# Performance work log

Measured on AMD Instinct MI355X. Metric: run time of the kernel, lower is better.

The kernel has to match this reference:

```python
import jax, jax.numpy as jnp
import numpy as np

B, IMG, P, CIN, D, L, H, HID = 64, 224, 16, 3, 768, 12, 12, 3072
HD = D // H                      # 64 head dim
N = (IMG // P) ** 2 + 1          # 197 tokens (cls + patches)
EQ = 1.0 / np.sqrt(D)            # EqualLinear scale (lr_mul=1)


def _ln(x):
    # LayerNorm(eps=1e-3, elementwise_affine=False)
    m = jnp.mean(x, axis=-1, keepdims=True)
    v = jnp.var(x, axis=-1, keepdims=True)
    return (x - m) * jax.lax.rsqrt(v + 1e-3)


def _smln(x, latent, gw, gb, bw, bb):
    # SelfModulatedLayerNorm: param-free LN then per-sample affine from latent
    gamma = (latent @ (gw * EQ).T + gb)[:, None, :]
    beta = (latent @ (bw * EQ).T + bb)[:, None, :]
    return _ln(x) * (1.0 + gamma) + beta


def _attention(x, qkvw, projw, projb):
    b, n, d = x.shape
    qkv = (x @ qkvw.T).reshape(b, n, 3, H, HD).transpose(2, 0, 3, 1, 4)  # [3,B,H,N,hd]
    q, k, v = qkv[0], qkv[1], qkv[2]
    attn = jax.nn.softmax(jnp.einsum('bhqd,bhkd->bhqk', q, k) * (HD ** -0.5), axis=-1)
    out = jnp.einsum('bhqk,bhkd->bhqd', attn, v).transpose(0, 2, 1, 3).reshape(b, n, d)
    return out @ projw.T + projb


def _forward(x, latent, conv_w, conv_b, cls_token, pos_embed,
             g1w, g1b, b1w, b1b, qkvw, projw, projb,
             g2w, g2b, b2w, b2b, fc1w, fc1b, fc2w, fc2b,
             gnw, gnb, bnw, bnb):
    b = x.shape[0]
    # PatchEmbed: conv stride=patch, flatten, transpose, sin activation
    feat = jax.lax.conv_general_dilated(
        x, conv_w, (P, P), 'VALID',
        dimension_numbers=('NCHW', 'OIHW', 'NCHW')) + conv_b[None, :, None, None]
    tok = jnp.sin(feat.reshape(b, D, -1).transpose(0, 2, 1))          # [B,196,D]
    tok = jnp.concatenate([jnp.broadcast_to(cls_token, (b, 1, D)), tok], axis=1)
    tok = tok + pos_embed                                             # [B,197,D]

    def block(t, p):
        (g1w_, g1b_, b1w_, b1b_, qkvw_, projw_, projb_,
         g2w_, g2b_, b2w_, b2b_, fc1w_, fc1b_, fc2w_, fc2b_) = p
        xn = _smln(t, latent, g1w_, g1b_, b1w_, b1b_)
        y = _attention(xn, qkvw_, projw_, projb_) + xn
        t = xn + y                       # source Block: x reassigned to norm1 output
        t = _smln(t, latent, g2w_, g2b_, b2w_, b2b_)
        h = jax.nn.gelu(t @ fc1w_.T + fc1b_, approximate=False)
        t = (h @ fc2w_.T + fc2b_) + t
        return t, None

    tok, _ = jax.lax.scan(block, tok, (g1w, g1b, b1w, b1b, qkvw, projw, projb,
                                       g2w, g2b, b2w, b2b, fc1w, fc1b, fc2w, fc2b))
    return _smln(tok, latent, gnw, gnb, bnw, bnb)


def setup_inputs() -> dict:
    key = jax.random.key(0)
    ks = jax.random.split(key, 20)
    r = lambda k, shape: 0.02 * jax.random.normal(k, shape, dtype=jnp.float32)
    z = lambda shape: jnp.zeros(shape, jnp.float32)
    return {
        'x': jax.random.normal(ks[0], (B, CIN, IMG, IMG), dtype=jnp.float32),
        'latent': jax.random.normal(ks[1], (B, D), dtype=jnp.float32),
        'conv_w': r(ks[2], (D, CIN, P, P)), 'conv_b': z((D,)),
        'cls_token': z((1, 1, D)), 'pos_embed': r(ks[3], (1, N, D)),
        'g1w': r(ks[4], (L, D, D)), 'g1b': z((L, D)),
        'b1w': r(ks[5], (L, D, D)), 'b1b': z((L, D)),
        'qkvw': r(ks[6], (L, 3 * D, D)),
        'projw': r(ks[7], (L, D, D)), 'projb': z((L, D)),
        'g2w': r(ks[8], (L, D, D)), 'g2b': z((L, D)),
        'b2w': r(ks[9], (L, D, D)), 'b2b': z((L, D)),
        'fc1w': r(ks[10], (L, HID, D)), 'fc1b': z((L, HID)),
        'fc2w': r(ks[11], (L, D, HID)), 'fc2b': z((L, D)),
        'gnw': r(ks[12], (D, D)), 'gnb': z((D,)),
        'bnw': r(ks[13], (D, D)), 'bnb': z((D,)),
    }


def reference(x, latent, conv_w, conv_b, cls_token, pos_embed,
              g1w, g1b, b1w, b1b, qkvw, projw, projb,
              g2w, g2b, b2w, b2b, fc1w, fc1b, fc2w, fc2b,
              gnw, gnb, bnw, bnb):
    return _forward(x, latent, conv_w, conv_b, cls_token, pos_embed,
                    g1w, g1b, b1w, b1b, qkvw, projw, projb,
                    g2w, g2b, b2w, b2b, fc1w, fc1b, fc2w, fc2b,
                    gnw, gnb, bnw, bnb)
```

## Files before the change

kernel.cpp:

```cpp
#include <hip/hip_runtime.h>

typedef unsigned short u16;
typedef __bf16 bf16x8 __attribute__((ext_vector_type(8)));
typedef unsigned short u16x8 __attribute__((ext_vector_type(8)));
typedef float f32x4 __attribute__((ext_vector_type(4)));

#define B_    64
#define NTOK  197
#define DIM   768
#define NH    12
#define LAY   12
#define HID_  3072
#define MROWS (B_*NTOK)

#define EPI_BF16  0
#define EPI_PROJ  2
#define EPI_GELU  3
#define EPI_FC2   4
#define EPI_PATCH 5

__device__ __forceinline__ u16 f2bf(float f) {
  unsigned u = __float_as_uint(f);
  u += 0x7FFFu + ((u >> 16) & 1u);
  return (u16)(u >> 16);
}
__device__ __forceinline__ float bf2f(u16 h) {
  return __uint_as_float(((unsigned)h) << 16);
}

__device__ __forceinline__ void gld_lds16(const void* g, void* l) {
  __builtin_amdgcn_global_load_lds(
      (const __attribute__((address_space(1))) void*)g,
      (__attribute__((address_space(3))) void*)l, 16, 0, 0);
}

__global__ void fill_k(float* __restrict__ o, float v, int n) {
  int i = blockIdx.x * blockDim.x + threadIdx.x;
  const int st = gridDim.x * blockDim.x;
  for (; i < n; i += st) o[i] = v;
}

__global__ void cvt_bf16(const float* __restrict__ in, u16* __restrict__ out, int n4) {
  int i = blockIdx.x * blockDim.x + threadIdx.x;
  const int st = gridDim.x * blockDim.x;
  for (; i < n4; i += st) {
    float4 v = ((const float4*)in)[i];
    ushort4 o;
    o.x = f2bf(v.x); o.y = f2bf(v.y); o.z = f2bf(v.z); o.w = f2bf(v.w);
    ((ushort4*)out)[i] = o;
  }
}

__global__ void cvt4_k(const float* __restrict__ s0, const float* __restrict__ s1,
                       const float* __restrict__ s2, const float* __restrict__ s3,
                       u16* __restrict__ d0, u16* __restrict__ d1,
                       u16* __restrict__ d2, u16* __restrict__ d3,
                       int n0, int n1, int n2, int n3)
{
  int i = blockIdx.x * blockDim.x + threadIdx.x;
  const int st = gridDim.x * blockDim.x;
  const int total = n0 + n1 + n2 + n3;
  for (; i < total; i += st) {
    const float* s; u16* d; int j = i;
    if (j < n0) { s = s0; d = d0; }
    else { j -= n0;
      if (j < n1) { s = s1; d = d1; }
      else { j -= n1;
        if (j < n2) { s = s2; d = d2; }
        else { j -= n2; s = s3; d = d3; } } }
    float4 v = ((const float4*)s)[j];
    ushort4 o;
    o.x = f2bf(v.x); o.y = f2bf(v.y); o.z = f2bf(v.z); o.w = f2bf(v.w);
    ((ushort4*)d)[j] = o;
  }
}

__global__ void im2col_k(const float* __restrict__ x, u16* __restrict__ out) {
  int i = blockIdx.x * blockDim.x + threadIdx.x;
  const int st = gridDim.x * blockDim.x;
  const int total = 12544 * 768;
  for (; i < total; i += st) {
    int row = i / 768, col = i - row * 768;
    int b = row / 196, pr = row - b * 196;
    int py = pr / 14, px = pr - py * 14;
    int cin = col >> 8, rr = col & 255;
    int ky = rr >> 4, kx = rr & 15;
    out[i] = f2bf(x[((b * 3 + cin) * 224 + py * 16 + ky) * 224 + px * 16 + kx]);
  }
}

__global__ void clspos_k(const float* __restrict__ cls, const float* __restrict__ pos,
                         float* __restrict__ t) {
  int i = blockIdx.x * blockDim.x + threadIdx.x;
  if (i >= B_ * DIM) return;
  int b = i / DIM, d = i - b * DIM;
  t[(size_t)b * NTOK * DIM + d] = cls[d] + pos[d];
}

__global__ __launch_bounds__(256)
void modk(const float* __restrict__ lat, const float* __restrict__ w,
          const float* __restrict__ bias, float* __restrict__ out, int ldb)
{
  __shared__ float ls[32][65];
  __shared__ float wsm[64][33];
  const int tid = threadIdx.x;
  const int mat = blockIdx.y;
  const int n0 = blockIdx.x * 64;
  const int nl = tid & 63;
  const int bg = tid >> 6;
  float acc[16];
  #pragma unroll
  for (int j = 0; j < 16; ++j) acc[j] = 0.f;
  for (int k0 = 0; k0 < 768; k0 += 32) {
    __syncthreads();
    #pragma unroll
    for (int i = 0; i < 8; ++i) {
      int idx = tid + i * 256;
      int rr = idx >> 5, kk = idx & 31;
      ls[kk][rr]  = lat[rr * 768 + k0 + kk];
      wsm[rr][kk] = w[((size_t)mat * 768 + n0 + rr) * 768 + k0 + kk];
    }
    __syncthreads();
    #pragma unroll 4
    for (int kk = 0; kk < 32; ++kk) {
      float wv = wsm[nl][kk];
      #pragma unroll
      for (int j = 0; j < 16; ++j)
        acc[j] += ls[kk][bg * 16 + j] * wv;
    }
  }
  const float EQS = 0.036084391824351615f;
  const float* bs = bias + (size_t)mat * 768 + n0;
  #pragma unroll
  for (int j = 0; j < 16; ++j) {
    int b = bg * 16 + j;
    out[(size_t)b * ldb + mat * 768 + n0 + nl] = acc[j] * EQS + bs[nl];
  }
}

__global__ __launch_bounds__(256)
void smln_k(const float* __restrict__ x,
            const float* __restrict__ gamma, const float* __restrict__ beta, int ldg,
            float* __restrict__ oF, u16* __restrict__ oB)
{
  const int row = blockIdx.x;
  const int tid = threadIdx.x;
  const float* xr = x + (size_t)row * DIM;
  float v0 = xr[tid], v1 = xr[tid + 256], v2 = xr[tid + 512];
  float s1 = v0 + v1 + v2;
  float s2 = v0 * v0 + v1 * v1 + v2 * v2;
  #pragma unroll
  for (int o = 32; o; o >>= 1) { s1 += __shfl_xor(s1, o); s2 += __shfl_xor(s2, o); }
  __shared__ float rs[8];
  const int lane = tid & 63, wv = tid >> 6;
  if (lane == 0) { rs[wv] = s1; rs[4 + wv] = s2; }
  __syncthreads();
  s1 = rs[0] + rs[1] + rs[2] + rs[3];
  s2 = rs[4] + rs[5] + rs[6] + rs[7];
  const float mean = s1 * (1.f / 768.f);
  const float var  = s2 * (1.f / 768.f) - mean * mean;
  const float rstd = rsqrtf(var + 1e-3f);
  const int b = row / NTOK;
  const float* g  = gamma + (size_t)b * ldg;
  const float* be = beta  + (size_t)b * ldg;
  const size_t base = (size_t)row * DIM;
  float vv[3] = {v0, v1, v2};
  #pragma unroll
  for (int j = 0; j < 3; ++j) {
    int d = tid + j * 256;
    float y = (vv[j] - mean) * rstd;
    y = y * (1.f + g[d]) + be[d];
    oF[base + d] = y;
    if (oB) oB[base + d] = f2bf(y);
  }
}

__global__ __launch_bounds__(256)
void attn_k(const u16* __restrict__ qkv, u16* __restrict__ ao)
{
  __shared__ u16 Ks[208 * 68];
  __shared__ u16 Vt[64 * 226];
  __shared__ u16 Ps[4][16 * 228];
  const int bh = blockIdx.x;
  const int b = bh / NH, h = bh - (bh / NH) * NH;
  const int tid = threadIdx.x;
  const int lane = tid & 63, wv = tid >> 6;
  const int lr = lane & 15, kg = lane >> 4;
  const size_t tb = (size_t)(b * NTOK) * 2304 + h * 64;

  for (int t = tid; t < 1576; t += 256) {
    int n = t >> 3, c = t & 7;
    *(u16x8*)&Ks[n * 68 + c * 8] =
        *(const u16x8*)&qkv[tb + (size_t)n * 2304 + 768 + c * 8];
  }
  for (int t = tid; t < 1576; t += 256) {
    int n = t >> 3, dc = t & 7;
    u16x8 v = *(const u16x8*)&qkv[tb + (size_t)n * 2304 + 1536 + dc * 8];
    #pragma unroll
    for (int j = 0; j < 8; ++j) Vt[(dc * 8 + j) * 226 + n] = v[j];
  }
  for (int i = tid; i < 11 * 68; i += 256) Ks[197 * 68 + i] = 0;
  for (int i = tid; i < 64 * 29; i += 256) {
    int d = i / 29, c = i - d * 29;
    Vt[d * 226 + 197 + c] = 0;
  }
  for (int i = tid; i < 4 * 16 * 20; i += 256) {
    int w = i / 320, rm = i - w * 320, r = rm / 20, c = rm - r * 20;
    Ps[w][r * 228 + 208 + c] = 0;
  }
  __syncthreads();

  const f32x4 z4 = {0.f, 0.f, 0.f, 0.f};
  u16* pw = Ps[wv];

  for (int qt = wv; qt < 13; qt += 4) {
    const int q0 = qt * 16;
    const int qrow = min(q0 + lr, 196);
    const bf16x8 aq0 = *(const bf16x8*)&qkv[tb + (size_t)qrow * 2304 + kg * 8];
    const bf16x8 aq1 = *(const bf16x8*)&qkv[tb + (size_t)qrow * 2304 + 32 + kg * 8];

    f32x4 acc[13];
    #pragma unroll
    for (int ct = 0; ct < 13; ++ct) acc[ct] = z4;
    #pragma unroll
    for (int ct = 0; ct < 13; ++ct) {
      const bf16x8 bk0 = *(const bf16x8*)&Ks[(ct * 16 + lr) * 68 + kg * 8];
      const bf16x8 bk1 = *(const bf16x8*)&Ks[(ct * 16 + lr) * 68 + 32 + kg * 8];
      acc[ct] = __builtin_amdgcn_mfma_f32_16x16x32_bf16(aq0, bk0, acc[ct], 0, 0, 0);
      acc[ct] = __builtin_amdgcn_mfma_f32_16x16x32_bf16(aq1, bk1, acc[ct], 0, 0, 0);
    }

    float mx[4], sm[4], inv[4];
    #pragma unroll
    for (int r = 0; r < 4; ++r) mx[r] = -1e30f;
    #pragma unroll
    for (int ct = 0; ct < 13; ++ct)
      #pragma unroll
      for (int r = 0; r < 4; ++r) {
        float s = acc[ct][r] * 0.125f;
        if (ct * 16 + lr >= 197) s = -1e30f;
        acc[ct][r] = s;
        mx[r] = fmaxf(mx[r], s);
      }
    #pragma unroll
    for (int o = 1; o < 16; o <<= 1)
      #pragma unroll
      for (int r = 0; r < 4; ++r) mx[r] = fmaxf(mx[r], __shfl_xor(mx[r], o));
    #pragma unroll
    for (int r = 0; r < 4; ++r) sm[r] = 0.f;
    #pragma unroll
    for (int ct = 0; ct < 13; ++ct)
      #pragma unroll
      for (int r = 0; r < 4; ++r) {
        float p = __expf(acc[ct][r] - mx[r]);
        acc[ct][r] = p;
        sm[r] += p;
      }
    #pragma unroll
    for (int o = 1; o < 16; o <<= 1)
      #pragma unroll
      for (int r = 0; r < 4; ++r) sm[r] += __shfl_xor(sm[r], o);
    #pragma unroll
    for (int r = 0; r < 4; ++r) inv[r] = 1.f / sm[r];

    #pragma unroll
    for (int ct = 0; ct < 13; ++ct)
      #pragma unroll
      for (int r = 0; r < 4; ++r)
        pw[(kg * 4 + r) * 228 + ct * 16 + lr] = f2bf(acc[ct][r]);
    asm volatile("s_waitcnt lgkmcnt(0)" ::: "memory");
    __builtin_amdgcn_sched_barrier(0);

    f32x4 accO[4];
    #pragma unroll
    for (int dt = 0; dt < 4; ++dt) accO[dt] = z4;
    #pragma unroll
    for (int kt = 0; kt < 7; ++kt) {
      const bf16x8 ap = *(const bf16x8*)&pw[lr * 228 + kt * 32 + kg * 8];
      #pragma unroll
      for (int dt = 0; dt < 4; ++dt) {
        const bf16x8 bv = *(const bf16x8*)&Vt[(dt * 16 + lr) * 226 + kt * 32 + kg * 8];
        accO[dt] = __builtin_amdgcn_mfma_f32_16x16x32_bf16(ap, bv, accO[dt], 0, 0, 0);
      }
    }

    #pragma unroll
    for (int r = 0; r < 4; ++r) {
      const int q = q0 + kg * 4 + r;
      if (q < NTOK) {
        const size_t base = ((size_t)(b * NTOK + q)) * DIM + h * 64;
        #pragma unroll
        for (int dt = 0; dt < 4; ++dt)
          ao[base + dt * 16 + lr] = f2bf(accO[dt][r] * inv[r]);
      }
    }
  }
}

template<int EPI>
__global__ __launch_bounds__(256)
void gemm_bt(const u16* __restrict__ A, int lda,
             const u16* __restrict__ Bw, int ldb,
             int M, int K, int gn,
             const float* __restrict__ bias,
             const float* __restrict__ res,
             float* __restrict__ outF, u16* __restrict__ outB, int ldo,
             const float* __restrict__ aux)
{
  __shared__ u16 SA[3][4096];
  __shared__ u16 SB[3][4096];
  const int tid = threadIdx.x;
  const int lane = tid & 63, wv = tid >> 6;
  const int lr = lane & 15, kg = lane >> 4;
  const int wm = wv >> 1, wn = wv & 1;

  const int nwg = gridDim.x;
  const int qq = nwg >> 3, rr2 = nwg & 7;
  const int xcd = blockIdx.x & 7, loc = blockIdx.x >> 3;
  const int v = (xcd < rr2 ? xcd * (qq + 1) : rr2 * (qq + 1) + (xcd - rr2) * qq) + loc;
  const int tm = v / gn, tn = v - tm * gn;

  const int c0 = tid, c1 = tid + 256;
  const int r0 = c0 >> 2, q0 = (c0 & 3) ^ (r0 & 3) ^ ((r0 >> 2) & 3);
  const int r1 = c1 >> 2, q1 = (c1 & 3) ^ (r1 & 3) ^ ((r1 >> 2) & 3);
  int am0 = tm * 128 + r0; if (am0 >= M) am0 = M - 1;
  int am1 = tm * 128 + r1; if (am1 >= M) am1 = M - 1;
  const u16* aS0 = A  + (size_t)am0 * lda + q0 * 8;
  const u16* aS1 = A  + (size_t)am1 * lda + q1 * 8;
  const u16* bS0 = Bw + (size_t)(tn * 128 + r0) * ldb + q0 * 8;
  const u16* bS1 = Bw + (size_t)(tn * 128 + r1) * ldb + q1 * 8;

  f32x4 acc[4][4];
  const f32x4 z = {0.f, 0.f, 0.f, 0.f};
  #pragma unroll
  for (int m = 0; m < 4; ++m)
    #pragma unroll
    for (int n = 0; n < 4; ++n) acc[m][n] = z;

#define STG(buf, ko) do { \
    u16* aD = &SA[buf][wv * 512]; u16* bD = &SB[buf][wv * 512]; \
    gld_lds16(aS0 + (ko), aD);        gld_lds16(aS1 + (ko), aD + 2048); \
    gld_lds16(bS0 + (ko), bD);        gld_lds16(bS1 + (ko), bD + 2048); \
  } while (0)

  const int KT = K >> 5;
  STG(0, 0);
  STG(1, 32);
  asm volatile("s_waitcnt vmcnt(4)" ::: "memory");
  __builtin_amdgcn_s_barrier();
  __builtin_amdgcn_sched_barrier(0);

  for (int t = 0; t < KT; ++t) {
    const int buf = t % 3;
    if (t) {
      asm volatile("s_waitcnt lgkmcnt(0)" ::: "memory");
      __builtin_amdgcn_sched_barrier(0);
      if (t + 1 < KT) asm volatile("s_waitcnt vmcnt(4)" ::: "memory");
      else            asm volatile("s_waitcnt vmcnt(0)" ::: "memory");
      __builtin_amdgcn_s_barrier();
      __builtin_amdgcn_sched_barrier(0);
    }
    if (t + 2 < KT) STG((t + 2) % 3, (t + 2) * 32);
    bf16x8 af[4], bfr[4];
    #pragma unroll
    for (int m = 0; m < 4; ++m) {
      int row = wm * 64 + m * 16 + lr;
      af[m] = *(const bf16x8*)&SA[buf][row * 32 + (((kg ^ row ^ (row >> 2)) & 3) << 3)];
    }
    #pragma unroll
    for (int n = 0; n < 4; ++n) {
      int row = wn * 64 + n * 16 + lr;
      bfr[n] = *(const bf16x8*)&SB[buf][row * 32 + (((kg ^ row ^ (row >> 2)) & 3) << 3)];
    }
    #pragma unroll
    for (int m = 0; m < 4; ++m)
      #pragma unroll
      for (int n = 0; n < 4; ++n)
        acc[m][n] = __builtin_amdgcn_mfma_f32_16x16x32_bf16(af[m], bfr[n], acc[m][n], 0, 0, 0);
  }
#undef STG
  __syncthreads();

  const int gr0 = tm * 128 + wm * 64;
  const int gc0 = tn * 128 + wn * 64;
  if constexpr (EPI == EPI_BF16 || EPI == EPI_GELU) {
    u16* T = (u16*)SA + wv * 1152;
    #pragma unroll
    for (int m = 0; m < 4; ++m) {
      #pragma unroll
      for (int n = 0; n < 4; ++n) {
        #pragma unroll
        for (int r = 0; r < 4; ++r) {
          float val = acc[m][n][r];
          if constexpr (EPI == EPI_GELU) {
            float u = val + bias[gc0 + n * 16 + lr];
            val = 0.5f * u * (1.f + erff(u * 0.70710678118654752f));
          }
          T[(kg * 4 + r) * 72 + n * 16 + lr] = f2bf(val);
        }
      }
      asm volatile("s_waitcnt lgkmcnt(0)" ::: "memory");
      __builtin_amdgcn_sched_barrier(0);
      #pragma unroll
      for (int half = 0; half < 2; ++half) {
        int row = (lane >> 3) + half * 8;
        int c8 = lane & 7;
        u16x8 vv = *(const u16x8*)&T[row * 72 + c8 * 8];
        int gr = gr0 + m * 16 + row;
        if (gr < M) *(u16x8*)&outB[(size_t)gr * ldo + gc0 + c8 * 8] = vv;
      }
      asm volatile("s_waitcnt lgkmcnt(0)" ::: "memory");
      __builtin_amdgcn_sched_barrier(0);
    }
  } else {
    float* T = (float*)SA + wv * 1088;
    #pragma unroll
    for (int m = 0; m < 4; ++m) {
      #pragma unroll
      for (int n = 0; n < 4; ++n)
        #pragma unroll
        for (int r = 0; r < 4; ++r)
          T[(kg * 4 + r) * 68 + n * 16 + lr] = acc[m][n][r];
      asm volatile("s_waitcnt lgkmcnt(0)" ::: "memory");
      __builtin_amdgcn_sched_barrier(0);
      #pragma unroll
      for (int qu = 0; qu < 4; ++qu) {
        int row = (lane >> 4) + qu * 4;
        int c4 = lane & 15;
        f32x4 vv = *(const f32x4*)&T[row * 68 + c4 * 4];
        int gr = gr0 + m * 16 + row;
        int gc = gc0 + c4 * 4;
        if (gr < M) {
          f32x4 bv = *(const f32x4*)&bias[gc];
          if constexpr (EPI == EPI_PROJ) {
            size_t o = (size_t)gr * ldo + gc;
            f32x4 rv = *(const f32x4*)&res[o];
            f32x4 ov = vv + bv + 2.f * rv;
            *(f32x4*)&outF[o] = ov;
          } else if constexpr (EPI == EPI_FC2) {
            size_t o = (size_t)gr * ldo + gc;
            f32x4 rv = *(const f32x4*)&res[o];
            f32x4 ov = vv + bv + rv;
            *(f32x4*)&outF[o] = ov;
          } else {
            int pb = gr / 196, pp = gr - pb * 196;
            size_t o = ((size_t)pb * NTOK + 1 + pp) * DIM + gc;
            f32x4 av = *(const f32x4*)&aux[(size_t)(1 + pp) * DIM + gc];
            f32x4 ov;
            #pragma unroll
            for (int j = 0; j < 4; ++j) ov[j] = sinf(vv[j] + bv[j]) + av[j];
            *(f32x4*)&outF[o] = ov;
          }
        }
      }
      asm volatile("s_waitcnt lgkmcnt(0)" ::: "memory");
      __builtin_amdgcn_sched_barrier(0);
    }
  }
}

extern "C" void kernel_launch(void* const* d_in, const int* in_sizes, int n_in,
                              void* d_out, int out_size, void* d_ws, size_t ws_size,
                              hipStream_t stream)
{
  (void)in_sizes; (void)n_in;
  const float* X     = (const float*)d_in[0];
  const float* LAT   = (const float*)d_in[1];
  const float* CONVW = (const float*)d_in[2];
  const float* CONVB = (const float*)d_in[3];
  const float* CLS   = (const float*)d_in[4];
  const float* POS   = (const float*)d_in[5];
  const float* G1W   = (const float*)d_in[6];
  const float* G1B   = (const float*)d_in[7];
  const float* B1W   = (const float*)d_in[8];
  const float* B1B   = (const float*)d_in[9];
  const float* QKVW  = (const float*)d_in[10];
  const float* PROJW = (const float*)d_in[11];
  const float* PROJB = (const float*)d_in[12];
  const float* G2W   = (const float*)d_in[13];
  const float* G2B   = (const float*)d_in[14];
  const float* B2W   = (const float*)d_in[15];
  const float* B2B   = (const float*)d_in[16];
  const float* FC1W  = (const float*)d_in[17];
  const float* FC1B  = (const float*)d_in[18];
  const float* FC2W  = (const float*)d_in[19];
  const float* FC2B  = (const float*)d_in[20];
  const float* GNW   = (const float*)d_in[21];
  const float* GNB   = (const float*)d_in[22];
  const float* BNW   = (const float*)d_in[23];
  const float* BNB   = (const float*)d_in[24];

  char* p = (char*)d_ws;
  auto carve = [&](size_t bytes) { char* r = p; p += (bytes + 255) & ~(size_t)255; return r; };

  char* Ubuf  = carve((size_t)MROWS * HID_ * 2);
  u16* patches = (u16*)Ubuf;
  u16* qkvb    = (u16*)Ubuf;
  u16* hb      = (u16*)Ubuf;
  u16* wconv  = (u16*)carve((size_t)768 * 768 * 2);
  u16* wqkv_l = (u16*)carve((size_t)2304 * 768 * 2);
  u16* wproj_l= (u16*)carve((size_t)768 * 768 * 2);
  u16* wfc1_l = (u16*)carve((size_t)3072 * 768 * 2);
  u16* wfc2_l = (u16*)carve((size_t)768 * 3072 * 2);
  float* tf   = (float*)carve((size_t)MROWS * 768 * 4);
  float* xnf  = (float*)carve((size_t)MROWS * 768 * 4);
  u16* xnb    = (u16*)carve((size_t)MROWS * 768 * 2);
  u16* aob    = (u16*)carve((size_t)MROWS * 768 * 2);
  float* gam1 = (float*)carve((size_t)B_ * 9216 * 4);
  float* bet1 = (float*)carve((size_t)B_ * 9216 * 4);
  float* gam2 = (float*)carve((size_t)B_ * 9216 * 4);
  float* bet2 = (float*)carve((size_t)B_ * 9216 * 4);
  float* gamN = (float*)carve((size_t)B_ * 768 * 4);
  float* betN = (float*)carve((size_t)B_ * 768 * 4);

  fill_k<<<1, 64, 0, stream>>>((float*)d_out, 1e9f, 1);
  if ((size_t)(p - (char*)d_ws) > ws_size) {
    fill_k<<<256, 256, 0, stream>>>((float*)d_out, 1e9f, out_size);
    return;
  }

  modk<<<dim3(12, 12), 256, 0, stream>>>(LAT, G1W, G1B, gam1, 9216);
  modk<<<dim3(12, 12), 256, 0, stream>>>(LAT, B1W, B1B, bet1, 9216);
  modk<<<dim3(12, 12), 256, 0, stream>>>(LAT, G2W, G2B, gam2, 9216);
  modk<<<dim3(12, 12), 256, 0, stream>>>(LAT, B2W, B2B, bet2, 9216);
  modk<<<dim3(12, 1),  256, 0, stream>>>(LAT, GNW, GNB, gamN, 768);
  modk<<<dim3(12, 1),  256, 0, stream>>>(LAT, BNW, BNB, betN, 768);

  {
    int n4 = 768 * 768 / 4;
    cvt_bf16<<<(n4 + 255) / 256, 256, 0, stream>>>(CONVW, wconv, n4);
  }
  im2col_k<<<4096, 256, 0, stream>>>(X, patches);
  gemm_bt<EPI_PATCH><<<98 * 6, 256, 0, stream>>>(patches, 768, wconv, 768, 12544, 768, 6,
                                                 CONVB, nullptr, tf, nullptr, 768, POS);
  clspos_k<<<(B_ * DIM + 255) / 256, 256, 0, stream>>>(CLS, POS, tf);

  const int n4_qkv = 2304 * 768 / 4, n4_pro = 768 * 768 / 4, n4_fc = 3072 * 768 / 4;
  for (int l = 0; l < LAY; ++l) {
    cvt4_k<<<4096, 256, 0, stream>>>(QKVW + (size_t)l * 2304 * 768, PROJW + (size_t)l * 768 * 768,
                                     FC1W + (size_t)l * 3072 * 768, FC2W + (size_t)l * 768 * 3072,
                                     wqkv_l, wproj_l, wfc1_l, wfc2_l,
                                     n4_qkv, n4_pro, n4_fc, n4_fc);
    smln_k<<<MROWS, 256, 0, stream>>>(tf, gam1 + l * 768, bet1 + l * 768, 9216, xnf, xnb);
    gemm_bt<EPI_BF16><<<99 * 18, 256, 0, stream>>>(xnb, 768, wqkv_l, 768, MROWS, 768, 18,
                                                   nullptr, nullptr, nullptr, qkvb, 2304, nullptr);
    attn_k<<<B_ * NH, 256, 0, stream>>>(qkvb, aob);
    gemm_bt<EPI_PROJ><<<99 * 6, 256, 0, stream>>>(aob, 768, wproj_l, 768, MROWS, 768, 6,
                                                  PROJB + l * 768, xnf, tf, nullptr, 768, nullptr);
    smln_k<<<MROWS, 256, 0, stream>>>(tf, gam2 + l * 768, bet2 + l * 768, 9216, xnf, xnb);
    gemm_bt<EPI_GELU><<<99 * 24, 256, 0, stream>>>(xnb, 768, wfc1_l, 768, MROWS, 768, 24,
                                                   FC1B + l * 3072, nullptr, nullptr, hb, 3072, nullptr);
    gemm_bt<EPI_FC2><<<99 * 6, 256, 0, stream>>>(hb, 3072, wfc2_l, 3072, MROWS, 3072, 6,
                                                 FC2B + l * 768, xnf, tf, nullptr, 768, nullptr);
  }
  smln_k<<<MROWS, 256, 0, stream>>>(tf, gamN, betN, 768, (float*)d_out, nullptr);
}
```

Measured before the change: 6.069 ms.

## Add 256x256-tile 8-wave GEMM for QKV and FC1, unroll triple-buffer loop

Adds a new GEMM kernel with 512 threads and 256x256 output tiles, a K-step of 64, double-buffered LDS and a phased schedule. The phases interleave A-fragment reads, global-to-LDS prefetch and MFMA bursts raised with s_setprio. The QKV and FC1 GEMMs use it, which cuts global/LDS traffic per FLOP and the number of workgroups. The existing 128x128 GEMM's main loop is also unrolled by three so buffer indices become compile-time constants instead of t%3. Risks: 256-row tiles waste work on the last M tile (12608 rows), fewer blocks means less occupancy and tail balance, and the 64KB of LDS per block limits co-residency. The unrolled loop steps by three and does not guard t < KT inside the body, so it relies on KT being a multiple of three, which holds for K=768 and K=3072.

```diff
diff --git a/kernel.cpp b/kernel.cpp
--- a/kernel.cpp
+++ b/kernel.cpp
@@ -298,6 +298,149 @@
 }
 
 template<int EPI>
+__global__ __launch_bounds__(512, 2)
+void gemm8(const u16* __restrict__ A, int lda,
+           const u16* __restrict__ Bw, int ldb,
+           int M, int K, int gn,
+           const float* __restrict__ bias,
+           u16* __restrict__ outB, int ldo)
+{
+  __shared__ u16 SA[2][16384];
+  __shared__ u16 SB[2][16384];
+  const int tid = threadIdx.x;
+  const int lane = tid & 63, wv = tid >> 6;
+  const int lr = lane & 15, kg = lane >> 4;
+  const int wm = wv >> 2, wn = wv & 3;
+
+  const int nwg = gridDim.x;
+  const int qq = nwg >> 3, rr2 = nwg & 7;
+  const int xcd = blockIdx.x & 7, loc = blockIdx.x >> 3;
+  const int v = (xcd < rr2 ? xcd * (qq + 1) : rr2 * (qq + 1) + (xcd - rr2) * qq) + loc;
+  const int tm = v / gn, tn = v - tm * gn;
+
+  const u16* aSrc[4];
+  const u16* bSrc[4];
+  #pragma unroll
+  for (int j = 0; j < 4; ++j) {
+    const int c = tid + j * 512;
+    const int r = c >> 3, q = (c & 7) ^ (r & 7);
+    int am = tm * 256 + r; if (am >= M) am = M - 1;
+    aSrc[j] = A  + (size_t)am * lda + q * 8;
+    bSrc[j] = Bw + (size_t)(tn * 256 + r) * ldb + q * 8;
+  }
+
+  f32x4 acc[8][4];
+  const f32x4 z = {0.f, 0.f, 0.f, 0.f};
+  #pragma unroll
+  for (int m = 0; m < 8; ++m)
+    #pragma unroll
+    for (int n = 0; n < 4; ++n) acc[m][n] = z;
+
+  const int KT = K >> 6;
+  #pragma unroll
+  for (int j = 0; j < 4; ++j) {
+    gld_lds16(aSrc[j], &SA[0][(tid + j * 512) * 8]);
+    gld_lds16(bSrc[j], &SB[0][(tid + j * 512) * 8]);
+  }
+  asm volatile("s_waitcnt vmcnt(0)" ::: "memory");
+  __builtin_amdgcn_s_barrier();
+  __builtin_amdgcn_sched_barrier(0);
+
+#define G8_PHASE(p) do { \
+    bf16x8 af[2][2]; \
+    _Pragma("unroll") \
+    for (int ks = 0; ks < 2; ++ks) \
+      _Pragma("unroll") \
+      for (int mm = 0; mm < 2; ++mm) { \
+        const int rrow = wm * 128 + ((p) * 2 + mm) * 16 + lr; \
+        af[ks][mm] = *(const bf16x8*)&sa[rrow * 64 + ((((ks * 4 + kg) ^ (rrow & 7))) << 3)]; \
+      } \
+    if ((p) < 2 && pf) { \
+      const int j0 = (p) * 2, j1 = (p) * 2 + 1; \
+      gld_lds16(aSrc[j0] + ko, &san[(tid + j0 * 512) * 8]); \
+      gld_lds16(aSrc[j1] + ko, &san[(tid + j1 * 512) * 8]); \
+      gld_lds16(bSrc[j0] + ko, &sbn[(tid + j0 * 512) * 8]); \
+      gld_lds16(bSrc[j1] + ko, &sbn[(tid + j1 * 512) * 8]); \
+    } \
+    __builtin_amdgcn_s_barrier(); \
+    asm volatile("s_waitcnt lgkmcnt(0)" ::: "memory"); \
+    __builtin_amdgcn_sched_barrier(0); \
+    __builtin_amdgcn_s_setprio(1); \
+    _Pragma("unroll") \
+    for (int ks = 0; ks < 2; ++ks) \
+      _Pragma("unroll") \
+      for (int mm = 0; mm < 2; ++mm) \
+        _Pragma("unroll") \
+        for (int n = 0; n < 4; ++n) \
+          acc[(p) * 2 + mm][n] = __builtin_amdgcn_mfma_f32_16x16x32_bf16( \
+              af[ks][mm], bfr[ks][n], acc[(p) * 2 + mm][n], 0, 0, 0); \
+    __builtin_amdgcn_s_setprio(0); \
+  } while (0)
+
+  for (int kt = 0; kt < KT; ++kt) {
+    const int bu = kt & 1;
+    const u16* sa = SA[bu];
+    const u16* sb = SB[bu];
+    u16* san = SA[bu ^ 1];
+    u16* sbn = SB[bu ^ 1];
+    const int ko = (kt + 1) * 64;
+    const bool pf = (kt + 1 < KT);
+
+    bf16x8 bfr[2][4];
+    #pragma unroll
+    for (int ks = 0; ks < 2; ++ks)
+      #pragma unroll
+      for (int n = 0; n < 4; ++n) {
+        const int rrow = wn * 64 + n * 16 + lr;
+        bfr[ks][n] = *(const bf16x8*)&sb[rrow * 64 + ((((ks * 4 + kg) ^ (rrow & 7))) << 3)];
+      }
+
+    G8_PHASE(0);
+    __builtin_amdgcn_s_barrier();
+    G8_PHASE(1);
+    __builtin_amdgcn_s_barrier();
+    G8_PHASE(2);
+    __builtin_amdgcn_s_barrier();
+    G8_PHASE(3);
+    if (pf) { asm volatile("s_waitcnt vmcnt(0)" ::: "memory"); }
+    __builtin_amdgcn_s_barrier();
+    __builtin_amdgcn_sched_barrier(0);
+  }
+#undef G8_PHASE
+
+  const int gr0 = tm * 256 + wm * 128;
+  const int gc0 = tn * 256 + wn * 64;
+  u16* T = (u16*)SA + wv * 1152;
+  #pragma unroll
+  for (int m = 0; m < 8; ++m) {
+    #pragma unroll
+    for (int n = 0; n < 4; ++n) {
+      #pragma unroll
+      for (int r = 0; r < 4; ++r) {
+        float val = acc[m][n][r];
+        if constexpr (EPI == EPI_GELU) {
+          float u = val + bias[gc0 + n * 16 + lr];
+          val = 0.5f * u * (1.f + erff(u * 0.70710678118654752f));
+        }
+        T[(kg * 4 + r) * 72 + n * 16 + lr] = f2bf(val);
+      }
+    }
+    asm volatile("s_waitcnt lgkmcnt(0)" ::: "memory");
+    __builtin_amdgcn_sched_barrier(0);
+    #pragma unroll
+    for (int half = 0; half < 2; ++half) {
+      int row = (lane >> 3) + half * 8;
+      int c8 = lane & 7;
+      u16x8 vv = *(const u16x8*)&T[row * 72 + c8 * 8];
+      int gr = gr0 + m * 16 + row;
+      if (gr < M) *(u16x8*)&outB[(size_t)gr * ldo + gc0 + c8 * 8] = vv;
+    }
+    asm volatile("s_waitcnt lgkmcnt(0)" ::: "memory");
+    __builtin_amdgcn_sched_barrier(0);
+  }
+}
+
+template<int EPI>
 __global__ __launch_bounds__(256)
 void gemm_bt(const u16* __restrict__ A, int lda,
              const u16* __restrict__ Bw, int ldb,
@@ -350,33 +493,37 @@
   __builtin_amdgcn_s_barrier();
   __builtin_amdgcn_sched_barrier(0);
 
-  for (int t = 0; t < KT; ++t) {
-    const int buf = t % 3;
-    if (t) {
-      asm volatile("s_waitcnt lgkmcnt(0)" ::: "memory");
-      __builtin_amdgcn_sched_barrier(0);
-      if (t + 1 < KT) asm volatile("s_waitcnt vmcnt(4)" ::: "memory");
-      else            asm volatile("s_waitcnt vmcnt(0)" ::: "memory");
-      __builtin_amdgcn_s_barrier();
-      __builtin_amdgcn_sched_barrier(0);
-    }
-    if (t + 2 < KT) STG((t + 2) % 3, (t + 2) * 32);
-    bf16x8 af[4], bfr[4];
-    #pragma unroll
-    for (int m = 0; m < 4; ++m) {
-      int row = wm * 64 + m * 16 + lr;
-      af[m] = *(const bf16x8*)&SA[buf][row * 32 + (((kg ^ row ^ (row >> 2)) & 3) << 3)];
-    }
-    #pragma unroll
-    for (int n = 0; n < 4; ++n) {
-      int row = wn * 64 + n * 16 + lr;
-      bfr[n] = *(const bf16x8*)&SB[buf][row * 32 + (((kg ^ row ^ (row >> 2)) & 3) << 3)];
-    }
-    #pragma unroll
-    for (int m = 0; m < 4; ++m)
-      #pragma unroll
-      for (int n = 0; n < 4; ++n)
-        acc[m][n] = __builtin_amdgcn_mfma_f32_16x16x32_bf16(af[m], bfr[n], acc[m][n], 0, 0, 0);
+  #pragma unroll 1
+  for (int t0 = 0; t0 < KT; t0 += 3) {
+    #pragma unroll
+    for (int u = 0; u < 3; ++u) {
+      const int t = t0 + u;
+      if (t) {
+        asm volatile("s_waitcnt lgkmcnt(0)" ::: "memory");
+        __builtin_amdgcn_sched_barrier(0);
+        if (t + 1 < KT) asm volatile("s_waitcnt vmcnt(4)" ::: "memory");
+        else            asm volatile("s_waitcnt vmcnt(0)" ::: "memory");
+        __builtin_amdgcn_s_barrier();
+        __builtin_amdgcn_sched_barrier(0);
+      }
+      if (t + 2 < KT) STG((u + 2) % 3, (t + 2) * 32);
+      bf16x8 af[4], bfr[4];
+      #pragma unroll
+      for (int m = 0; m < 4; ++m) {
+        int row = wm * 64 + m * 16 + lr;
+        af[m] = *(const bf16x8*)&SA[u][row * 32 + (((kg ^ row ^ (row >> 2)) & 3) << 3)];
+      }
+      #pragma unroll
+      for (int n = 0; n < 4; ++n) {
+        int row = wn * 64 + n * 16 + lr;
+        bfr[n] = *(const bf16x8*)&SB[u][row * 32 + (((kg ^ row ^ (row >> 2)) & 3) << 3)];
+      }
+      #pragma unroll
+      for (int m = 0; m < 4; ++m)
+        #pragma unroll
+        for (int n = 0; n < 4; ++n)
+          acc[m][n] = __builtin_amdgcn_mfma_f32_16x16x32_bf16(af[m], bfr[n], acc[m][n], 0, 0, 0);
+    }
   }
 #undef STG
   __syncthreads();
@@ -542,14 +689,14 @@
                                      wqkv_l, wproj_l, wfc1_l, wfc2_l,
                                      n4_qkv, n4_pro, n4_fc, n4_fc);
     smln_k<<<MROWS, 256, 0, stream>>>(tf, gam1 + l * 768, bet1 + l * 768, 9216, xnf, xnb);
-    gemm_bt<EPI_BF16><<<99 * 18, 256, 0, stream>>>(xnb, 768, wqkv_l, 768, MROWS, 768, 18,
-                                                   nullptr, nullptr, nullptr, qkvb, 2304, nullptr);
+    gemm8<EPI_BF16><<<50 * 9, 512, 0, stream>>>(xnb, 768, wqkv_l, 768, MROWS, 768, 9,
+                                                nullptr, qkvb, 2304);
     attn_k<<<B_ * NH, 256, 0, stream>>>(qkvb, aob);
     gemm_bt<EPI_PROJ><<<99 * 6, 256, 0, stream>>>(aob, 768, wproj_l, 768, MROWS, 768, 6,
                                                   PROJB + l * 768, xnf, tf, nullptr, 768, nullptr);
     smln_k<<<MROWS, 256, 0, stream>>>(tf, gam2 + l * 768, bet2 + l * 768, 9216, xnf, xnb);
-    gemm_bt<EPI_GELU><<<99 * 24, 256, 0, stream>>>(xnb, 768, wfc1_l, 768, MROWS, 768, 24,
-                                                   FC1B + l * 3072, nullptr, nullptr, hb, 3072, nullptr);
+    gemm8<EPI_GELU><<<50 * 12, 512, 0, stream>>>(xnb, 768, wfc1_l, 768, MROWS, 768, 12,
+                                                 FC1B + l * 3072, hb, 3072);
     gemm_bt<EPI_FC2><<<99 * 6, 256, 0, stream>>>(hb, 3072, wfc2_l, 3072, MROWS, 3072, 6,
                                                  FC2B + l * 768, xnf, tf, nullptr, 768, nullptr);
   }
```

Measured after the change: 7.652 ms. 26.1% more time.

## Drop fp32 norm output, read bf16 residual, add 4-stage GEMM pipeline option

Applied to the files above, without the earlier changes.

The layer-norm kernels stop writing the fp32 normalized activations, and the proj and fc2 epilogues read the residual from the bf16 copy instead. This cuts activation memory traffic per layer. The GEMM gains a templated pipeline depth, with the K loop unrolled by depth, and the QKV and FC1 GEMMs use 4 LDS stages. The risks are lower residual precision from the bf16 rounding, and higher LDS use, which may lower occupancy.

```diff
diff --git a/kernel.cpp b/kernel.cpp
--- a/kernel.cpp
+++ b/kernel.cpp
@@ -170,7 +170,7 @@
     int d = tid + j * 256;
     float y = (vv[j] - mean) * rstd;
     y = y * (1.f + g[d]) + be[d];
-    oF[base + d] = y;
+    if (oF) oF[base + d] = y;
     if (oB) oB[base + d] = f2bf(y);
   }
 }
@@ -297,18 +297,18 @@
   }
 }
 
-template<int EPI>
+template<int EPI, int DEPTH>
 __global__ __launch_bounds__(256)
 void gemm_bt(const u16* __restrict__ A, int lda,
              const u16* __restrict__ Bw, int ldb,
              int M, int K, int gn,
              const float* __restrict__ bias,
-             const float* __restrict__ res,
+             const u16* __restrict__ res,
              float* __restrict__ outF, u16* __restrict__ outB, int ldo,
              const float* __restrict__ aux)
 {
-  __shared__ u16 SA[3][4096];
-  __shared__ u16 SB[3][4096];
+  __shared__ u16 SA[DEPTH][4096];
+  __shared__ u16 SB[DEPTH][4096];
   const int tid = threadIdx.x;
   const int lane = tid & 63, wv = tid >> 6;
   const int lr = lane & 15, kg = lane >> 4;
@@ -344,39 +344,50 @@
   } while (0)
 
   const int KT = K >> 5;
-  STG(0, 0);
-  STG(1, 32);
-  asm volatile("s_waitcnt vmcnt(4)" ::: "memory");
+  #pragma unroll
+  for (int d = 0; d < DEPTH - 1; ++d) STG(d, d * 32);
+  if constexpr (DEPTH == 4) { asm volatile("s_waitcnt vmcnt(8)" ::: "memory"); }
+  else                      { asm volatile("s_waitcnt vmcnt(4)" ::: "memory"); }
   __builtin_amdgcn_s_barrier();
   __builtin_amdgcn_sched_barrier(0);
 
-  for (int t = 0; t < KT; ++t) {
-    const int buf = t % 3;
-    if (t) {
-      asm volatile("s_waitcnt lgkmcnt(0)" ::: "memory");
-      __builtin_amdgcn_sched_barrier(0);
-      if (t + 1 < KT) asm volatile("s_waitcnt vmcnt(4)" ::: "memory");
-      else            asm volatile("s_waitcnt vmcnt(0)" ::: "memory");
-      __builtin_amdgcn_s_barrier();
-      __builtin_amdgcn_sched_barrier(0);
-    }
-    if (t + 2 < KT) STG((t + 2) % 3, (t + 2) * 32);
-    bf16x8 af[4], bfr[4];
-    #pragma unroll
-    for (int m = 0; m < 4; ++m) {
-      int row = wm * 64 + m * 16 + lr;
-      af[m] = *(const bf16x8*)&SA[buf][row * 32 + (((kg ^ row ^ (row >> 2)) & 3) << 3)];
-    }
-    #pragma unroll
-    for (int n = 0; n < 4; ++n) {
-      int row = wn * 64 + n * 16 + lr;
-      bfr[n] = *(const bf16x8*)&SB[buf][row * 32 + (((kg ^ row ^ (row >> 2)) & 3) << 3)];
-    }
-    #pragma unroll
-    for (int m = 0; m < 4; ++m)
-      #pragma unroll
-      for (int n = 0; n < 4; ++n)
-        acc[m][n] = __builtin_amdgcn_mfma_f32_16x16x32_bf16(af[m], bfr[n], acc[m][n], 0, 0, 0);
+  #pragma unroll 1
+  for (int t0 = 0; t0 < KT; t0 += DEPTH) {
+    #pragma unroll
+    for (int u = 0; u < DEPTH; ++u) {
+      const int t = t0 + u;
+      if (t) {
+        asm volatile("s_waitcnt lgkmcnt(0)" ::: "memory");
+        __builtin_amdgcn_sched_barrier(0);
+        if (t + DEPTH - 2 < KT) {
+          if constexpr (DEPTH == 4) { asm volatile("s_waitcnt vmcnt(8)" ::: "memory"); }
+          else                      { asm volatile("s_waitcnt vmcnt(4)" ::: "memory"); }
+        } else if (t + 1 < KT) {
+          asm volatile("s_waitcnt vmcnt(4)" ::: "memory");
+        } else {
+          asm volatile("s_waitcnt vmcnt(0)" ::: "memory");
+        }
+        __builtin_amdgcn_s_barrier();
+        __builtin_amdgcn_sched_barrier(0);
+      }
+      if (t + DEPTH - 1 < KT) STG((u + DEPTH - 1) % DEPTH, (t + DEPTH - 1) * 32);
+      bf16x8 af[4], bfr[4];
+      #pragma unroll
+      for (int m = 0; m < 4; ++m) {
+        int row = wm * 64 + m * 16 + lr;
+        af[m] = *(const bf16x8*)&SA[u][row * 32 + (((kg ^ row ^ (row >> 2)) & 3) << 3)];
+      }
+      #pragma unroll
+      for (int n = 0; n < 4; ++n) {
+        int row = wn * 64 + n * 16 + lr;
+        bfr[n] = *(const bf16x8*)&SB[u][row * 32 + (((kg ^ row ^ (row >> 2)) & 3) << 3)];
+      }
+      #pragma unroll
+      for (int m = 0; m < 4; ++m)
+        #pragma unroll
+        for (int n = 0; n < 4; ++n)
+          acc[m][n] = __builtin_amdgcn_mfma_f32_16x16x32_bf16(af[m], bfr[n], acc[m][n], 0, 0, 0);
+    }
   }
 #undef STG
   __syncthreads();
@@ -434,13 +445,21 @@
           f32x4 bv = *(const f32x4*)&bias[gc];
           if constexpr (EPI == EPI_PROJ) {
             size_t o = (size_t)gr * ldo + gc;
-            f32x4 rv = *(const f32x4*)&res[o];
-            f32x4 ov = vv + bv + 2.f * rv;
+            ushort4 rv = *(const ushort4*)&res[o];
+            f32x4 ov;
+            ov[0] = vv[0] + bv[0] + 2.f * bf2f(rv.x);
+            ov[1] = vv[1] + bv[1] + 2.f * bf2f(rv.y);
+            ov[2] = vv[2] + bv[2] + 2.f * bf2f(rv.z);
+            ov[3] = vv[3] + bv[3] + 2.f * bf2f(rv.w);
             *(f32x4*)&outF[o] = ov;
           } else if constexpr (EPI == EPI_FC2) {
             size_t o = (size_t)gr * ldo + gc;
-            f32x4 rv = *(const f32x4*)&res[o];
-            f32x4 ov = vv + bv + rv;
+            ushort4 rv = *(const ushort4*)&res[o];
+            f32x4 ov;
+            ov[0] = vv[0] + bv[0] + bf2f(rv.x);
+            ov[1] = vv[1] + bv[1] + bf2f(rv.y);
+            ov[2] = vv[2] + bv[2] + bf2f(rv.z);
+            ov[3] = vv[3] + bv[3] + bf2f(rv.w);
             *(f32x4*)&outF[o] = ov;
           } else {
             int pb = gr / 196, pp = gr - pb * 196;
@@ -503,7 +522,6 @@
   u16* wfc1_l = (u16*)carve((size_t)3072 * 768 * 2);
   u16* wfc2_l = (u16*)carve((size_t)768 * 3072 * 2);
   float* tf   = (float*)carve((size_t)MROWS * 768 * 4);
-  float* xnf  = (float*)carve((size_t)MROWS * 768 * 4);
   u16* xnb    = (u16*)carve((size_t)MROWS * 768 * 2);
   u16* aob    = (u16*)carve((size_t)MROWS * 768 * 2);
   float* gam1 = (float*)carve((size_t)B_ * 9216 * 4);
@@ -531,8 +549,8 @@
     cvt_bf16<<<(n4 + 255) / 256, 256, 0, stream>>>(CONVW, wconv, n4);
   }
   im2col_k<<<4096, 256, 0, stream>>>(X, patches);
-  gemm_bt<EPI_PATCH><<<98 * 6, 256, 0, stream>>>(patches, 768, wconv, 768, 12544, 768, 6,
-                                                 CONVB, nullptr, tf, nullptr, 768, POS);
+  gemm_bt<EPI_PATCH, 3><<<98 * 6, 256, 0, stream>>>(patches, 768, wconv, 768, 12544, 768, 6,
+                                                    CONVB, nullptr, tf, nullptr, 768, POS);
   clspos_k<<<(B_ * DIM + 255) / 256, 256, 0, stream>>>(CLS, POS, tf);
 
   const int n4_qkv = 2304 * 768 / 4, n4_pro = 768 * 768 / 4, n4_fc = 3072 * 768 / 4;
@@ -541,17 +559,17 @@
                                      FC1W + (size_t)l * 3072 * 768, FC2W + (size_t)l * 768 * 3072,
                                      wqkv_l, wproj_l, wfc1_l, wfc2_l,
                                      n4_qkv, n4_pro, n4_fc, n4_fc);
-    smln_k<<<MROWS, 256, 0, stream>>>(tf, gam1 + l * 768, bet1 + l * 768, 9216, xnf, xnb);
-    gemm_bt<EPI_BF16><<<99 * 18, 256, 0, stream>>>(xnb, 768, wqkv_l, 768, MROWS, 768, 18,
-                                                   nullptr, nullptr, nullptr, qkvb, 2304, nullptr);
+    smln_k<<<MROWS, 256, 0, stream>>>(tf, gam1 + l * 768, bet1 + l * 768, 9216, nullptr, xnb);
+    gemm_bt<EPI_BF16, 4><<<99 * 18, 256, 0, stream>>>(xnb, 768, wqkv_l, 768, MROWS, 768, 18,
+                                                      nullptr, nullptr, nullptr, qkvb, 2304, nullptr);
     attn_k<<<B_ * NH, 256, 0, stream>>>(qkvb, aob);
-    gemm_bt<EPI_PROJ><<<99 * 6, 256, 0, stream>>>(aob, 768, wproj_l, 768, MROWS, 768, 6,
-                                                  PROJB + l * 768, xnf, tf, nullptr, 768, nullptr);
-    smln_k<<<MROWS, 256, 0, stream>>>(tf, gam2 + l * 768, bet2 + l * 768, 9216, xnf, xnb);
-    gemm_bt<EPI_GELU><<<99 * 24, 256, 0, stream>>>(xnb, 768, wfc1_l, 768, MROWS, 768, 24,
-                                                   FC1B + l * 3072, nullptr, nullptr, hb, 3072, nullptr);
-    gemm_bt<EPI_FC2><<<99 * 6, 256, 0, stream>>>(hb, 3072, wfc2_l, 3072, MROWS, 3072, 6,
-                                                 FC2B + l * 768, xnf, tf, nullptr, 768, nullptr);
+    gemm_bt<EPI_PROJ, 3><<<99 * 6, 256, 0, stream>>>(aob, 768, wproj_l, 768, MROWS, 768, 6,
+                                                     PROJB + l * 768, xnb, tf, nullptr, 768, nullptr);
+    smln_k<<<MROWS, 256, 0, stream>>>(tf, gam2 + l * 768, bet2 + l * 768, 9216, nullptr, xnb);
+    gemm_bt<EPI_GELU, 4><<<99 * 24, 256, 0, stream>>>(xnb, 768, wfc1_l, 768, MROWS, 768, 24,
+                                                      FC1B + l * 3072, nullptr, nullptr, hb, 3072, nullptr);
+    gemm_bt<EPI_FC2, 3><<<99 * 6, 256, 0, stream>>>(hb, 3072, wfc2_l, 3072, MROWS, 3072, 6,
+                                                    FC2B + l * 768, xnb, tf, nullptr, 768, nullptr);
   }
   smln_k<<<MROWS, 256, 0, stream>>>(tf, gamN, betN, 768, (float*)d_out, nullptr);
 }
```

Measured after the change: 7.063 ms. +16.4%, slower.
